# Performance work log

Measured on AMD Instinct MI355X. Metric: run time of the kernel, lower is better.

## Reference

```python
import jax, jax.numpy as jnp
import numpy as np
import math

N_BITS = 3
N_EMBD = 2048
N_HEAD = 16
B, T = 1, 2048


def fake_quant_act(x, bits=N_BITS):
    # Brevitas Int8ActPerTensorFloat at 3 bits: signed, non-narrow range [-4, 3]
    qmin, qmax = -(2 ** (bits - 1)), 2 ** (bits - 1) - 1
    s = jax.lax.stop_gradient(jnp.max(jnp.abs(x))) / (2 ** (bits - 1))
    q = jnp.clip(jnp.round(x / s), qmin, qmax) * s
    return x + jax.lax.stop_gradient(q - x)  # STE


def fake_quant_weight(w, bits=N_BITS):
    # Int8WeightPerTensorFloat, narrow_range=True at 3 bits: range [-3, 3]
    qmax = 2 ** (bits - 1) - 1
    s = jax.lax.stop_gradient(jnp.max(jnp.abs(w))) / qmax
    q = jnp.clip(jnp.round(w / s), -qmax, qmax) * s
    return w + jax.lax.stop_gradient(q - w)  # STE


def setup_inputs() -> dict:
    key = jax.random.key(0)
    ks = jax.random.split(key, 7)
    W_STD = 0.02  # GPT-style init keeps exp(att) in range (own_softmax has no max-subtract)
    x = jax.random.normal(ks[0], (B, T, N_EMBD), dtype=jnp.float32)
    W1 = jax.random.normal(ks[1], (N_EMBD, N_EMBD), dtype=jnp.float32) * W_STD
    W2 = jax.random.normal(ks[2], (N_EMBD, N_EMBD), dtype=jnp.float32) * W_STD
    W3 = jax.random.normal(ks[3], (N_EMBD, N_EMBD), dtype=jnp.float32) * W_STD
    b1 = jax.random.normal(ks[4], (N_EMBD,), dtype=jnp.float32) * W_STD
    b2 = jax.random.normal(ks[5], (N_EMBD,), dtype=jnp.float32) * W_STD
    b3 = jax.random.normal(ks[6], (N_EMBD,), dtype=jnp.float32) * W_STD
    return {"x": x, "W1": W1, "b1": b1, "W2": W2, "b2": b2, "W3": W3, "b3": b3}


def reference(x, W1, b1, W2, b2, W3, b3):
    hs = N_EMBD // N_HEAD
    xq = fake_quant_act(x)  # quant_inp
    q = xq @ fake_quant_weight(W1).T + b1  # c_attn1
    k = xq @ fake_quant_weight(W2).T + b2  # c_attn2
    v = xq @ fake_quant_weight(W3).T + b3  # c_attn3
    # [B,T,C] -> [B,nh,T,hs]
    q = q.reshape(B, T, N_HEAD, hs).transpose(0, 2, 1, 3)
    k = k.reshape(B, T, N_HEAD, hs).transpose(0, 2, 1, 3)
    v = v.reshape(B, T, N_HEAD, hs).transpose(0, 2, 1, 3)
    att = jnp.einsum("bhqd,bhkd->bhqk", q, k) * (1.0 / math.sqrt(hs))
    # own_softmax: exp normalized over dim=1 == the HEAD axis (faithful to source; no mask)
    e = jnp.exp(att)
    att = e / jnp.sum(e, axis=1, keepdims=True)
    # attn_dropout p=0 -> identity; c_proj never applied in forward
    y = jnp.einsum("bhqk,bhkd->bhqd", att, v)  # [B,nh,T,hs]
    return y
```

## Files before the change

### kernel.cpp

```cpp
#include <hip/hip_runtime.h>
#include <hip/hip_bf16.h>

typedef short bf16x8 __attribute__((ext_vector_type(8)));
typedef float f32x4 __attribute__((ext_vector_type(4)));
typedef unsigned short u16;

constexpr int TOKS = 2048;
constexpr int EMB  = 2048;
constexpr int NH   = 16;
constexpr int HS   = 128;
constexpr float RSQ = 0.08838834764831845f;

constexpr size_t OFF_SCAL = 0;
constexpr size_t OFF_QX   = 1024;
constexpr size_t SZ_MAT   = (size_t)TOKS * EMB * 2;
constexpr size_t OFF_QW   = OFF_QX + SZ_MAT;
constexpr size_t OFF_Q    = OFF_QW + 3 * SZ_MAT;
constexpr size_t OFF_K    = OFF_Q + SZ_MAT;
constexpr size_t OFF_V    = OFF_K + SZ_MAT;
constexpr size_t OFF_VT   = OFF_V + SZ_MAT;
constexpr size_t OFF_DEN  = OFF_VT + SZ_MAT;
constexpr size_t OFF_DEN0 = OFF_QX;
constexpr size_t OFF_DEN1 = OFF_QX + (size_t)TOKS * TOKS * 4;

#define VMCNT(n) asm volatile("s_waitcnt vmcnt(" #n ")" ::: "memory")
#define LGKM0()  asm volatile("s_waitcnt lgkmcnt(0)" ::: "memory")
#define BAR()    do { asm volatile("" ::: "memory"); __builtin_amdgcn_s_barrier(); asm volatile("" ::: "memory"); } while (0)

__device__ __forceinline__ u16 f2b(float f) {
  unsigned u = __float_as_uint(f);
  unsigned r = (u + 0x7fffu + ((u >> 16) & 1u)) >> 16;
  return (u16)r;
}

__device__ __forceinline__ void gload16(const void* g, void* l) {
  __builtin_amdgcn_global_load_lds(
      (const __attribute__((address_space(1))) unsigned int*)g,
      (__attribute__((address_space(3))) unsigned int*)l, 16, 0, 0);
}

__global__ void k_init(int* scal) {
  if (threadIdx.x < 4) scal[threadIdx.x] = 0;
}

__global__ void k_absmax(const float* __restrict__ x, const float* __restrict__ w1,
                         const float* __restrict__ w2, const float* __restrict__ w3,
                         int* scal) {
  const float* src = (blockIdx.y == 0) ? x : (blockIdx.y == 1) ? w1 : (blockIdx.y == 2) ? w2 : w3;
  const float4* s4 = (const float4*)src;
  int idx = blockIdx.x * 256 + threadIdx.x;
  float m = 0.f;
  for (int i = 0; i < 16; ++i) {
    float4 v = s4[idx + i * 65536];
    m = fmaxf(m, fmaxf(fmaxf(fabsf(v.x), fabsf(v.y)), fmaxf(fabsf(v.z), fabsf(v.w))));
  }
  for (int o = 32; o; o >>= 1) m = fmaxf(m, __shfl_down(m, o));
  __shared__ float red[4];
  if ((threadIdx.x & 63) == 0) red[threadIdx.x >> 6] = m;
  __syncthreads();
  if (threadIdx.x == 0) {
    m = fmaxf(fmaxf(red[0], red[1]), fmaxf(red[2], red[3]));
    atomicMax(&scal[blockIdx.y], __float_as_int(m));
  }
}

__global__ void k_quant(const float* __restrict__ x, const float* __restrict__ w1,
                        const float* __restrict__ w2, const float* __restrict__ w3,
                        u16* qx, u16* qw, const int* scal) {
  int a = blockIdx.y;
  const float* src = (a == 0) ? x : (a == 1) ? w1 : (a == 2) ? w2 : w3;
  u16* dst = (a == 0) ? qx : qw + (size_t)(a - 1) * TOKS * EMB;
  float mx = __int_as_float(scal[a]);
  float s = (a == 0) ? mx * 0.25f : mx / 3.0f;
  float lo = (a == 0) ? -4.f : -3.f;
  const float hi = 3.f;
  int idx = blockIdx.x * 256 + threadIdx.x;
  for (int i = 0; i < 16; ++i) {
    int j = idx + i * 65536;
    float4 v = ((const float4*)src)[j];
    ushort4 o;
    o.x = f2b(fminf(fmaxf(rintf(v.x / s), lo), hi));
    o.y = f2b(fminf(fmaxf(rintf(v.y / s), lo), hi));
    o.z = f2b(fminf(fmaxf(rintf(v.z / s), lo), hi));
    o.w = f2b(fminf(fmaxf(rintf(v.w / s), lo), hi));
    ((ushort4*)dst)[j] = o;
  }
}

__global__ __launch_bounds__(256, 3) void k_gemm(const u16* __restrict__ qx, const u16* __restrict__ qw,
    const float* __restrict__ b1, const float* __restrict__ b2, const float* __restrict__ b3,
    const int* __restrict__ scal, u16* qo, u16* ko, u16* vo) {
  int z = blockIdx.z;
  const u16* W = qw + (size_t)z * TOKS * EMB;
  const float* bias = (z == 0) ? b1 : (z == 1) ? b2 : b3;
  u16* out = (z == 0) ? qo : (z == 1) ? ko : vo;
  float sx = __int_as_float(scal[0]) * 0.25f;
  float sw = __int_as_float(scal[1 + z]) / 3.0f;
  float alpha = sx * sw;
  float extra = (z == 0) ? RSQ : 1.0f;
  int t0 = blockIdx.y * 128, o0 = blockIdx.x * 128;
  __shared__ __align__(16) u16 As[128 * 64];
  __shared__ __align__(16) u16 Bs[128 * 64];
  int tid = threadIdx.x, lane = tid & 63, wid = tid >> 6;
  int mh = (wid >> 1) * 64, nh = (wid & 1) * 64;
  f32x4 acc[4][4] = {};
  const char* Ab = (const char*)qx;
  const char* Bb = (const char*)W;
  for (int kk = 0; kk < 32; ++kk) {
#pragma unroll
    for (int p = 0; p < 4; ++p) {
      int L = p * 4096 + tid * 16;
      int r = L >> 7;
      int s = ((L >> 4) & 7) ^ (r & 7);
      gload16(Ab + (size_t)(t0 + r) * 4096 + kk * 128 + s * 16,
              (char*)As + p * 4096 + wid * 1024);
      gload16(Bb + (size_t)(o0 + r) * 4096 + kk * 128 + s * 16,
              (char*)Bs + p * 4096 + wid * 1024);
    }
    __syncthreads();
#pragma unroll
    for (int ks = 0; ks < 2; ++ks) {
      bf16x8 af[4], bfr[4];
#pragma unroll
      for (int m = 0; m < 4; ++m) {
        int row = mh + m * 16 + (lane & 15);
        int sl = (ks * 4 + (lane >> 4)) ^ (row & 7);
        af[m] = *(const bf16x8*)((const char*)As + row * 128 + sl * 16);
      }
#pragma unroll
      for (int n = 0; n < 4; ++n) {
        int row = nh + n * 16 + (lane & 15);
        int sl = (ks * 4 + (lane >> 4)) ^ (row & 7);
        bfr[n] = *(const bf16x8*)((const char*)Bs + row * 128 + sl * 16);
      }
#pragma unroll
      for (int m = 0; m < 4; ++m)
#pragma unroll
        for (int n = 0; n < 4; ++n)
          acc[m][n] = __builtin_amdgcn_mfma_f32_16x16x32_bf16(af[m], bfr[n], acc[m][n], 0, 0, 0);
    }
    __syncthreads();
  }
#pragma unroll
  for (int m = 0; m < 4; ++m)
#pragma unroll
    for (int n = 0; n < 4; ++n) {
      int ocol = o0 + nh + n * 16 + (lane & 15);
      float bb = bias[ocol];
#pragma unroll
      for (int r = 0; r < 4; ++r) {
        int trow = t0 + mh + m * 16 + (lane >> 4) * 4 + r;
        float v = (acc[m][n][r] * alpha + bb) * extra;
        out[(size_t)trow * EMB + ocol] = f2b(v);
      }
    }
}

__global__ void k_transpose(const u16* __restrict__ v, u16* vt) {
  int h = blockIdx.z, d0 = blockIdx.y * 64, t0 = blockIdx.x * 64;
  __shared__ u16 tile[64][65];
  int tid = threadIdx.x;
  for (int i = 0; i < 16; ++i) {
    int idx = i * 256 + tid, r = idx >> 6, c = idx & 63;
    tile[r][c] = v[(size_t)(t0 + r) * EMB + h * HS + d0 + c];
  }
  __syncthreads();
  for (int i = 0; i < 16; ++i) {
    int idx = i * 256 + tid, r = idx >> 6, c = idx & 63;
    vt[(size_t)(h * HS + d0 + r) * TOKS + t0 + c] = tile[c][r];
  }
}

__global__ __launch_bounds__(256, 2) void k_denom(const u16* __restrict__ q, const u16* __restrict__ k,
                                                  float* __restrict__ den0, float* __restrict__ den1) {
  int kt0 = blockIdx.x * 128, qt0 = blockIdx.y * 128, hg = blockIdx.z;
  float* den = hg ? den1 : den0;
  __shared__ __align__(16) u16 As[2][128 * 64];
  __shared__ __align__(16) u16 Bs[2][128 * 64];
  int tid = threadIdx.x, lane = tid & 63, wid = tid >> 6;
  int mh = (wid >> 1) * 64, nh = (wid & 1) * 64;
  f32x4 acc[4][4] = {}, dd[4][4] = {};
  auto stage = [&](int st, int buf) {
    int cb = hg * 2048 + st * 128;
#pragma unroll
    for (int p = 0; p < 4; ++p) {
      int L = p * 4096 + tid * 16;
      int r = L >> 7;
      int s = ((L >> 4) & 7) ^ (r & 7);
      gload16((const char*)q + (size_t)(qt0 + r) * 4096 + cb + s * 16,
              (char*)As[buf] + p * 4096 + wid * 1024);
      gload16((const char*)k + (size_t)(kt0 + r) * 4096 + cb + s * 16,
              (char*)Bs[buf] + p * 4096 + wid * 1024);
    }
  };
  stage(0, 0);
  for (int st = 0; st < 16; ++st) {
    int cur = st & 1;
    if (st < 15) { stage(st + 1, cur ^ 1); VMCNT(8); } else { VMCNT(0); }
    BAR();
#pragma unroll
    for (int ks = 0; ks < 2; ++ks) {
      bf16x8 af[4], bfr[4];
#pragma unroll
      for (int m = 0; m < 4; ++m) {
        int row = mh + m * 16 + (lane & 15);
        int sl = (ks * 4 + (lane >> 4)) ^ (row & 7);
        af[m] = *(const bf16x8*)((const char*)As[cur] + row * 128 + sl * 16);
      }
#pragma unroll
      for (int n = 0; n < 4; ++n) {
        int row = nh + n * 16 + (lane & 15);
        int sl = (ks * 4 + (lane >> 4)) ^ (row & 7);
        bfr[n] = *(const bf16x8*)((const char*)Bs[cur] + row * 128 + sl * 16);
      }
#pragma unroll
      for (int m = 0; m < 4; ++m)
#pragma unroll
        for (int n = 0; n < 4; ++n)
          acc[m][n] = __builtin_amdgcn_mfma_f32_16x16x32_bf16(af[m], bfr[n], acc[m][n], 0, 0, 0);
    }
    BAR();
    if (st & 1) {
#pragma unroll
      for (int m = 0; m < 4; ++m)
#pragma unroll
        for (int n = 0; n < 4; ++n) {
#pragma unroll
          for (int r = 0; r < 4; ++r) dd[m][n][r] += __expf(acc[m][n][r]);
          acc[m][n] = f32x4{0.f, 0.f, 0.f, 0.f};
        }
    }
  }
#pragma unroll
  for (int m = 0; m < 4; ++m)
#pragma unroll
    for (int n = 0; n < 4; ++n)
#pragma unroll
      for (int r = 0; r < 4; ++r) {
        int qrow = qt0 + mh + m * 16 + (lane >> 4) * 4 + r;
        int kcol = kt0 + nh + n * 16 + (lane & 15);
        den[(size_t)qrow * TOKS + kcol] = dd[m][n][r];
      }
}

__global__ void k_recip(const float* __restrict__ a, const float* __restrict__ b,
                        float* __restrict__ o) {
  int i = blockIdx.x * 256 + threadIdx.x;
  const float4* a4 = (const float4*)a;
  const float4* b4 = (const float4*)b;
  float4* o4 = (float4*)o;
#pragma unroll
  for (int j = 0; j < 4; ++j) {
    int t = i + j * 262144;
    float4 va = a4[t], vb = b4[t];
    float4 r;
    r.x = 1.0f / (va.x + vb.x);
    r.y = 1.0f / (va.y + vb.y);
    r.z = 1.0f / (va.z + vb.z);
    r.w = 1.0f / (va.w + vb.w);
    o4[t] = r;
  }
}

__global__ __launch_bounds__(256, 2) void k_attn(const u16* __restrict__ q, const u16* __restrict__ k,
                                                 const u16* __restrict__ vt, const float* __restrict__ invden,
                                                 float* __restrict__ out) {
  int qt0 = blockIdx.x * 64, h = blockIdx.y;
  __shared__ __align__(16) u16 Ks[2][64 * 128];
  __shared__ __align__(16) u16 Vs[2][128 * 64];
  __shared__ __align__(16) u16 Ps[64 * 64];
  int tid = threadIdx.x, lane = tid & 63, wid = tid >> 6;

  auto stageKV = [&](int kb, int buf) {
#pragma unroll
    for (int p = 0; p < 4; ++p) {
      int L = p * 4096 + tid * 16;
      int r = L >> 8;
      int s = ((L >> 4) & 15) ^ (r & 7);
      gload16((const char*)k + (size_t)(kb * 64 + r) * 4096 + h * 256 + s * 16,
              (char*)Ks[buf] + p * 4096 + wid * 1024);
    }
#pragma unroll
    for (int p = 0; p < 4; ++p) {
      int L = p * 4096 + tid * 16;
      int r = L >> 7;
      int s = ((L >> 4) & 7) ^ (r & 7);
      gload16((const char*)vt + (size_t)(h * HS + r) * 4096 + kb * 128 + s * 16,
              (char*)Vs[buf] + p * 4096 + wid * 1024);
    }
  };
  stageKV(0, 0);
  bf16x8 qf[4][4];
#pragma unroll
  for (int m = 0; m < 4; ++m)
#pragma unroll
    for (int c = 0; c < 4; ++c)
      qf[m][c] = *(const bf16x8*)(q + (size_t)(qt0 + m * 16 + (lane & 15)) * EMB
                                  + h * HS + c * 32 + (lane >> 4) * 8);
  f32x4 yacc[4][2] = {};
  const float* dinv = invden + (size_t)qt0 * TOKS;
  for (int kb = 0; kb < 32; ++kb) {
    int cur = kb & 1;
    if (kb < 31) { stageKV(kb + 1, cur ^ 1); VMCNT(12); } else { VMCNT(4); }
    BAR();
    f32x4 pacc[4] = {};
#pragma unroll
    for (int c = 0; c < 4; ++c) {
      int row = wid * 16 + (lane & 15);
      int sl = (c * 4 + (lane >> 4)) ^ (row & 7);
      bf16x8 bk = *(const bf16x8*)((const char*)Ks[cur] + row * 256 + sl * 16);
#pragma unroll
      for (int m = 0; m < 4; ++m)
        pacc[m] = __builtin_amdgcn_mfma_f32_16x16x32_bf16(qf[m][c], bk, pacc[m], 0, 0, 0);
    }
#pragma unroll
    for (int m = 0; m < 4; ++m)
#pragma unroll
      for (int r = 0; r < 4; ++r) {
        int qr = m * 16 + (lane >> 4) * 4 + r;
        int kc = kb * 64 + wid * 16 + (lane & 15);
        float e = __expf(pacc[m][r]) * dinv[(size_t)qr * TOKS + kc];
        int col = wid * 16 + (lane & 15);
        int psl = (col >> 3) ^ (qr & 7);
        *(u16*)((char*)Ps + qr * 128 + psl * 16 + (col & 7) * 2) = f2b(e);
      }
    if (kb < 31) { VMCNT(8); } else { VMCNT(0); }
    LGKM0();
    BAR();
#pragma unroll
    for (int ks = 0; ks < 2; ++ks) {
      bf16x8 pa[4], bv[2];
#pragma unroll
      for (int m = 0; m < 4; ++m) {
        int row = m * 16 + (lane & 15);
        int sl = (ks * 4 + (lane >> 4)) ^ (row & 7);
        pa[m] = *(const bf16x8*)((const char*)Ps + row * 128 + sl * 16);
      }
#pragma unroll
      for (int j = 0; j < 2; ++j) {
        int row = wid * 32 + j * 16 + (lane & 15);
        int sl = (ks * 4 + (lane >> 4)) ^ (row & 7);
        bv[j] = *(const bf16x8*)((const char*)Vs[cur] + row * 128 + sl * 16);
      }
#pragma unroll
      for (int m = 0; m < 4; ++m)
#pragma unroll
        for (int j = 0; j < 2; ++j)
          yacc[m][j] = __builtin_amdgcn_mfma_f32_16x16x32_bf16(pa[m], bv[j], yacc[m][j], 0, 0, 0);
    }
    BAR();
  }
#pragma unroll
  for (int m = 0; m < 4; ++m)
#pragma unroll
    for (int j = 0; j < 2; ++j)
#pragma unroll
      for (int r = 0; r < 4; ++r) {
        int trow = qt0 + m * 16 + (lane >> 4) * 4 + r;
        int dcol = wid * 32 + j * 16 + (lane & 15);
        out[(size_t)(h * TOKS + trow) * HS + dcol] = yacc[m][j][r];
      }
}

extern "C" void kernel_launch(void* const* d_in, const int* in_sizes, int n_in,
                              void* d_out, int out_size, void* d_ws, size_t ws_size,
                              hipStream_t stream) {
  const float* x  = (const float*)d_in[0];
  const float* W1 = (const float*)d_in[1];
  const float* b1 = (const float*)d_in[2];
  const float* W2 = (const float*)d_in[3];
  const float* b2 = (const float*)d_in[4];
  const float* W3 = (const float*)d_in[5];
  const float* b3 = (const float*)d_in[6];
  char* ws = (char*)d_ws;
  int*   scal   = (int*)(ws + OFF_SCAL);
  u16*   qx     = (u16*)(ws + OFF_QX);
  u16*   qw     = (u16*)(ws + OFF_QW);
  u16*   qo     = (u16*)(ws + OFF_Q);
  u16*   ko     = (u16*)(ws + OFF_K);
  u16*   vo     = (u16*)(ws + OFF_V);
  u16*   vt     = (u16*)(ws + OFF_VT);
  float* den0   = (float*)(ws + OFF_DEN0);
  float* den1   = (float*)(ws + OFF_DEN1);
  float* invden = (float*)(ws + OFF_DEN);
  float* y      = (float*)d_out;

  hipLaunchKernelGGL(k_init, dim3(1), dim3(64), 0, stream, scal);
  hipLaunchKernelGGL(k_absmax, dim3(256, 4), dim3(256), 0, stream, x, W1, W2, W3, scal);
  hipLaunchKernelGGL(k_quant, dim3(256, 4), dim3(256), 0, stream, x, W1, W2, W3, qx, qw, scal);
  hipLaunchKernelGGL(k_gemm, dim3(16, 16, 3), dim3(256), 0, stream,
                     qx, qw, b1, b2, b3, scal, qo, ko, vo);
  hipLaunchKernelGGL(k_transpose, dim3(32, 2, 16), dim3(256), 0, stream, vo, vt);
  hipLaunchKernelGGL(k_denom, dim3(16, 16, 2), dim3(256), 0, stream, qo, ko, den0, den1);
  hipLaunchKernelGGL(k_recip, dim3(1024), dim3(256), 0, stream, den0, den1, invden);
  hipLaunchKernelGGL(k_attn, dim3(32, 16), dim3(256), 0, stream, qo, ko, vt, invden, y);
}
```

Baseline: 191.9 us.

## Fuse head-axis denominator and reciprocal into one full-width denom kernel

k_denom now covers all 16 heads in one block over the full 2048 channels and writes the reciprocal directly. This removes the split den0/den1 buffers and the separate k_recip pass with its extra 48MB of traffic. k_attn swaps the MFMA operand order so each lane holds four consecutive key columns. That lets it read invden as float4 and pack P with v_cvt_pk_bf16_f32 into 8-byte LDS stores. The change also adds s_setprio around the MFMA sections, flattens the grids so heads are the fastest-varying index, and raises denom occupancy to 3 blocks per CU, at the cost of a smaller 128x64 tile with more K-loop stages.

```diff
diff --git a/kernel.cpp b/kernel.cpp
--- a/kernel.cpp
+++ b/kernel.cpp
@@ -20,8 +20,6 @@
 constexpr size_t OFF_V    = OFF_K + SZ_MAT;
 constexpr size_t OFF_VT   = OFF_V + SZ_MAT;
 constexpr size_t OFF_DEN  = OFF_VT + SZ_MAT;
-constexpr size_t OFF_DEN0 = OFF_QX;
-constexpr size_t OFF_DEN1 = OFF_QX + (size_t)TOKS * TOKS * 4;
 
 #define VMCNT(n) asm volatile("s_waitcnt vmcnt(" #n ")" ::: "memory")
 #define LGKM0()  asm volatile("s_waitcnt lgkmcnt(0)" ::: "memory")
@@ -31,6 +29,12 @@
   unsigned u = __float_as_uint(f);
   unsigned r = (u + 0x7fffu + ((u >> 16) & 1u)) >> 16;
   return (u16)r;
+}
+
+__device__ __forceinline__ unsigned cvtpk(float a, float b) {
+  unsigned r;
+  asm("v_cvt_pk_bf16_f32 %0, %1, %2" : "=v"(r) : "v"(a), "v"(b));
+  return r;
 }
 
 __device__ __forceinline__ void gload16(const void* g, void* l) {
@@ -171,60 +175,68 @@
   }
 }
 
-__global__ __launch_bounds__(256, 2) void k_denom(const u16* __restrict__ q, const u16* __restrict__ k,
-                                                  float* __restrict__ den0, float* __restrict__ den1) {
-  int kt0 = blockIdx.x * 128, qt0 = blockIdx.y * 128, hg = blockIdx.z;
-  float* den = hg ? den1 : den0;
-  __shared__ __align__(16) u16 As[2][128 * 64];
-  __shared__ __align__(16) u16 Bs[2][128 * 64];
+__global__ __launch_bounds__(256, 3) void k_denom(const u16* __restrict__ q, const u16* __restrict__ k,
+                                                  float* __restrict__ invden) {
+  int bid = blockIdx.x;
+  int qy = bid & 15, kx = bid >> 4;
+  int qt0 = qy * 128, kt0 = kx * 64;
+  __shared__ __align__(16) u16 Qs[2][128 * 64];
+  __shared__ __align__(16) u16 Ksm[2][64 * 64];
   int tid = threadIdx.x, lane = tid & 63, wid = tid >> 6;
-  int mh = (wid >> 1) * 64, nh = (wid & 1) * 64;
-  f32x4 acc[4][4] = {}, dd[4][4] = {};
+  int wq = (wid >> 1) * 64, wk = (wid & 1) * 32;
+  f32x4 acc[4][2] = {}, dd[4][2] = {};
   auto stage = [&](int st, int buf) {
-    int cb = hg * 2048 + st * 128;
 #pragma unroll
     for (int p = 0; p < 4; ++p) {
       int L = p * 4096 + tid * 16;
       int r = L >> 7;
       int s = ((L >> 4) & 7) ^ (r & 7);
-      gload16((const char*)q + (size_t)(qt0 + r) * 4096 + cb + s * 16,
-              (char*)As[buf] + p * 4096 + wid * 1024);
-      gload16((const char*)k + (size_t)(kt0 + r) * 4096 + cb + s * 16,
-              (char*)Bs[buf] + p * 4096 + wid * 1024);
+      gload16((const char*)q + (size_t)(qt0 + r) * 4096 + st * 128 + s * 16,
+              (char*)Qs[buf] + p * 4096 + wid * 1024);
+    }
+#pragma unroll
+    for (int p = 0; p < 2; ++p) {
+      int L = p * 4096 + tid * 16;
+      int r = L >> 7;
+      int s = ((L >> 4) & 7) ^ (r & 7);
+      gload16((const char*)k + (size_t)(kt0 + r) * 4096 + st * 128 + s * 16,
+              (char*)Ksm[buf] + p * 4096 + wid * 1024);
     }
   };
   stage(0, 0);
-  for (int st = 0; st < 16; ++st) {
+  for (int st = 0; st < 32; ++st) {
     int cur = st & 1;
-    if (st < 15) { stage(st + 1, cur ^ 1); VMCNT(8); } else { VMCNT(0); }
-    BAR();
+    if (st < 31) { stage(st + 1, cur ^ 1); VMCNT(6); } else { VMCNT(0); }
+    BAR();
+    __builtin_amdgcn_s_setprio(1);
 #pragma unroll
     for (int ks = 0; ks < 2; ++ks) {
-      bf16x8 af[4], bfr[4];
+      bf16x8 af[4], bfr[2];
 #pragma unroll
       for (int m = 0; m < 4; ++m) {
-        int row = mh + m * 16 + (lane & 15);
-        int sl = (ks * 4 + (lane >> 4)) ^ (row & 7);
-        af[m] = *(const bf16x8*)((const char*)As[cur] + row * 128 + sl * 16);
-      }
-#pragma unroll
-      for (int n = 0; n < 4; ++n) {
-        int row = nh + n * 16 + (lane & 15);
-        int sl = (ks * 4 + (lane >> 4)) ^ (row & 7);
-        bfr[n] = *(const bf16x8*)((const char*)Bs[cur] + row * 128 + sl * 16);
-      }
-#pragma unroll
-      for (int m = 0; m < 4; ++m)
-#pragma unroll
-        for (int n = 0; n < 4; ++n)
+        int row = wq + m * 16 + (lane & 15);
+        int sl = (ks * 4 + (lane >> 4)) ^ (row & 7);
+        af[m] = *(const bf16x8*)((const char*)Qs[cur] + row * 128 + sl * 16);
+      }
+#pragma unroll
+      for (int n = 0; n < 2; ++n) {
+        int row = wk + n * 16 + (lane & 15);
+        int sl = (ks * 4 + (lane >> 4)) ^ (row & 7);
+        bfr[n] = *(const bf16x8*)((const char*)Ksm[cur] + row * 128 + sl * 16);
+      }
+#pragma unroll
+      for (int m = 0; m < 4; ++m)
+#pragma unroll
+        for (int n = 0; n < 2; ++n)
           acc[m][n] = __builtin_amdgcn_mfma_f32_16x16x32_bf16(af[m], bfr[n], acc[m][n], 0, 0, 0);
     }
+    __builtin_amdgcn_s_setprio(0);
     BAR();
     if (st & 1) {
 #pragma unroll
       for (int m = 0; m < 4; ++m)
 #pragma unroll
-        for (int n = 0; n < 4; ++n) {
+        for (int n = 0; n < 2; ++n) {
 #pragma unroll
           for (int r = 0; r < 4; ++r) dd[m][n][r] += __expf(acc[m][n][r]);
           acc[m][n] = f32x4{0.f, 0.f, 0.f, 0.f};
@@ -234,38 +246,20 @@
 #pragma unroll
   for (int m = 0; m < 4; ++m)
 #pragma unroll
-    for (int n = 0; n < 4; ++n)
+    for (int n = 0; n < 2; ++n)
 #pragma unroll
       for (int r = 0; r < 4; ++r) {
-        int qrow = qt0 + mh + m * 16 + (lane >> 4) * 4 + r;
-        int kcol = kt0 + nh + n * 16 + (lane & 15);
-        den[(size_t)qrow * TOKS + kcol] = dd[m][n][r];
-      }
-}
-
-__global__ void k_recip(const float* __restrict__ a, const float* __restrict__ b,
-                        float* __restrict__ o) {
-  int i = blockIdx.x * 256 + threadIdx.x;
-  const float4* a4 = (const float4*)a;
-  const float4* b4 = (const float4*)b;
-  float4* o4 = (float4*)o;
-#pragma unroll
-  for (int j = 0; j < 4; ++j) {
-    int t = i + j * 262144;
-    float4 va = a4[t], vb = b4[t];
-    float4 r;
-    r.x = 1.0f / (va.x + vb.x);
-    r.y = 1.0f / (va.y + vb.y);
-    r.z = 1.0f / (va.z + vb.z);
-    r.w = 1.0f / (va.w + vb.w);
-    o4[t] = r;
-  }
+        int qrow = qt0 + wq + m * 16 + (lane >> 4) * 4 + r;
+        int kcol = kt0 + wk + n * 16 + (lane & 15);
+        invden[(size_t)qrow * TOKS + kcol] = 1.0f / dd[m][n][r];
+      }
 }
 
 __global__ __launch_bounds__(256, 2) void k_attn(const u16* __restrict__ q, const u16* __restrict__ k,
                                                  const u16* __restrict__ vt, const float* __restrict__ invden,
                                                  float* __restrict__ out) {
-  int qt0 = blockIdx.x * 64, h = blockIdx.y;
+  int bid = blockIdx.x;
+  int h = bid & 15, qt0 = (bid >> 4) * 64;
   __shared__ __align__(16) u16 Ks[2][64 * 128];
   __shared__ __align__(16) u16 Vs[2][128 * 64];
   __shared__ __align__(16) u16 Ps[64 * 64];
@@ -304,6 +298,7 @@
     if (kb < 31) { stageKV(kb + 1, cur ^ 1); VMCNT(12); } else { VMCNT(4); }
     BAR();
     f32x4 pacc[4] = {};
+    __builtin_amdgcn_s_setprio(1);
 #pragma unroll
     for (int c = 0; c < 4; ++c) {
       int row = wid * 16 + (lane & 15);
@@ -311,30 +306,35 @@
       bf16x8 bk = *(const bf16x8*)((const char*)Ks[cur] + row * 256 + sl * 16);
 #pragma unroll
       for (int m = 0; m < 4; ++m)
-        pacc[m] = __builtin_amdgcn_mfma_f32_16x16x32_bf16(qf[m][c], bk, pacc[m], 0, 0, 0);
-    }
-#pragma unroll
-    for (int m = 0; m < 4; ++m)
-#pragma unroll
-      for (int r = 0; r < 4; ++r) {
-        int qr = m * 16 + (lane >> 4) * 4 + r;
-        int kc = kb * 64 + wid * 16 + (lane & 15);
-        float e = __expf(pacc[m][r]) * dinv[(size_t)qr * TOKS + kc];
-        int col = wid * 16 + (lane & 15);
-        int psl = (col >> 3) ^ (qr & 7);
-        *(u16*)((char*)Ps + qr * 128 + psl * 16 + (col & 7) * 2) = f2b(e);
-      }
+        pacc[m] = __builtin_amdgcn_mfma_f32_16x16x32_bf16(bk, qf[m][c], pacc[m], 0, 0, 0);
+    }
+    __builtin_amdgcn_s_setprio(0);
+#pragma unroll
+    for (int m = 0; m < 4; ++m) {
+      int qr = m * 16 + (lane & 15);
+      float4 dv = *(const float4*)&dinv[(size_t)qr * TOKS + kb * 64 + wid * 16 + (lane >> 4) * 4];
+      float e0 = __expf(pacc[m][0]) * dv.x;
+      float e1 = __expf(pacc[m][1]) * dv.y;
+      float e2 = __expf(pacc[m][2]) * dv.z;
+      float e3 = __expf(pacc[m][3]) * dv.w;
+      uint2 pk;
+      pk.x = cvtpk(e0, e1);
+      pk.y = cvtpk(e2, e3);
+      int kby = wid * 32 + (lane >> 4) * 8;
+      *(uint2*)((char*)Ps + qr * 128 + (kby ^ ((qr & 7) << 4))) = pk;
+    }
     if (kb < 31) { VMCNT(8); } else { VMCNT(0); }
     LGKM0();
     BAR();
+    __builtin_amdgcn_s_setprio(1);
 #pragma unroll
     for (int ks = 0; ks < 2; ++ks) {
       bf16x8 pa[4], bv[2];
 #pragma unroll
       for (int m = 0; m < 4; ++m) {
         int row = m * 16 + (lane & 15);
-        int sl = (ks * 4 + (lane >> 4)) ^ (row & 7);
-        pa[m] = *(const bf16x8*)((const char*)Ps + row * 128 + sl * 16);
+        int off = (ks * 64 + (lane >> 4) * 16) ^ ((row & 7) << 4);
+        pa[m] = *(const bf16x8*)((const char*)Ps + row * 128 + off);
       }
 #pragma unroll
       for (int j = 0; j < 2; ++j) {
@@ -348,6 +348,7 @@
         for (int j = 0; j < 2; ++j)
           yacc[m][j] = __builtin_amdgcn_mfma_f32_16x16x32_bf16(pa[m], bv[j], yacc[m][j], 0, 0, 0);
     }
+    __builtin_amdgcn_s_setprio(0);
     BAR();
   }
 #pragma unroll
@@ -380,8 +381,6 @@
   u16*   ko     = (u16*)(ws + OFF_K);
   u16*   vo     = (u16*)(ws + OFF_V);
   u16*   vt     = (u16*)(ws + OFF_VT);
-  float* den0   = (float*)(ws + OFF_DEN0);
-  float* den1   = (float*)(ws + OFF_DEN1);
   float* invden = (float*)(ws + OFF_DEN);
   float* y      = (float*)d_out;
 
@@ -391,7 +390,6 @@
   hipLaunchKernelGGL(k_gemm, dim3(16, 16, 3), dim3(256), 0, stream,
                      qx, qw, b1, b2, b3, scal, qo, ko, vo);
   hipLaunchKernelGGL(k_transpose, dim3(32, 2, 16), dim3(256), 0, stream, vo, vt);
-  hipLaunchKernelGGL(k_denom, dim3(16, 16, 2), dim3(256), 0, stream, qo, ko, den0, den1);
-  hipLaunchKernelGGL(k_recip, dim3(1024), dim3(256), 0, stream, den0, den1, invden);
-  hipLaunchKernelGGL(k_attn, dim3(32, 16), dim3(256), 0, stream, qo, ko, vt, invden, y);
-}
+  hipLaunchKernelGGL(k_denom, dim3(512), dim3(256), 0, stream, qo, ko, invden);
+  hipLaunchKernelGGL(k_attn, dim3(512), dim3(256), 0, stream, qo, ko, vt, invden, y);
+}
```

Measured after the change: 207.5 us. 1.08x slower.
